# Kernel optimization log

Measured on AMD Instinct MI355X. Metric: run time of the kernel, lower is better.

## Reference

```python
import jax, jax.numpy as jnp
import numpy as np

N_NODES = 50000
N_EDGES = 800000
IN_FEATS = 256
N_HEADS = 4
OUT_FEATS = 32
NEG_SLOPE = 0.2


def setup_inputs() -> dict:
    key = jax.random.key(0)
    k_feat, k_src, k_dst, k_fc, k_al, k_ar, k_res = jax.random.split(key, 7)
    feat = jax.random.normal(k_feat, (N_NODES, IN_FEATS), dtype=jnp.float32)
    src = jax.random.randint(k_src, (N_EDGES,), 0, N_NODES)
    dst = jax.random.randint(k_dst, (N_EDGES,), 0, N_NODES)
    # xavier-normal-ish scales
    s_fc = (2.0 / (IN_FEATS + N_HEADS * OUT_FEATS)) ** 0.5
    W_fc = jax.random.normal(k_fc, (N_HEADS * OUT_FEATS, IN_FEATS), dtype=jnp.float32) * s_fc
    s_a = (2.0 / (1 + N_HEADS * OUT_FEATS)) ** 0.5
    attn_l = jax.random.normal(k_al, (N_HEADS, OUT_FEATS), dtype=jnp.float32) * s_a
    attn_r = jax.random.normal(k_ar, (N_HEADS, OUT_FEATS), dtype=jnp.float32) * s_a
    W_res = jax.random.normal(k_res, (N_HEADS * OUT_FEATS, IN_FEATS), dtype=jnp.float32) * s_fc
    return {"feat": feat, "src": src, "dst": dst, "W_fc": W_fc,
            "attn_l": attn_l, "attn_r": attn_r, "W_res": W_res}


def reference(feat, src, dst, W_fc, attn_l, attn_r, W_res):
    N = feat.shape[0]
    H, D = attn_l.shape
    ones_e = jnp.ones(src.shape[0], dtype=feat.dtype)

    # projection: [N, H, D]
    h = (feat @ W_fc.T).reshape(N, H, D)
    feat_dst = h  # dst features are pre-norm (torch code aliases before * norm)

    # symmetric norm on source side: out_degree^-0.5
    out_deg = jax.ops.segment_sum(ones_e, src, num_segments=N)
    feat_src = h * (jnp.clip(out_deg, 1.0) ** -0.5)[:, None, None]

    # per-node attention halves -> per-edge score, leaky relu
    el = jnp.einsum('nhd,hd->nh', feat_src, attn_l)  # [N, H]
    er = jnp.einsum('nhd,hd->nh', feat_dst, attn_r)  # [N, H]
    e = jax.nn.leaky_relu(el[src] + er[dst], NEG_SLOPE)  # [E, H]

    # edge_softmax over incoming edges of each dst node
    emax = jax.ops.segment_max(e, dst, num_segments=N)
    emax = jnp.where(jnp.isfinite(emax), emax, 0.0)  # guard empty segments
    ex = jnp.exp(e - emax[dst])
    denom = jax.ops.segment_sum(ex, dst, num_segments=N)
    a = ex / denom[dst]  # [E, H]

    # weighted scatter-sum of messages: u_mul_e + sum
    msg = feat_src[src] * a[:, :, None]  # [E, H, D]
    rst = jax.ops.segment_sum(msg, dst, num_segments=N)  # [N, H, D]

    # symmetric norm on destination side: in_degree^0.5
    in_deg = jax.ops.segment_sum(ones_e, dst, num_segments=N)
    rst = rst * jnp.sqrt(jnp.clip(in_deg, 1.0))[:, None, None]

    # residual projection
    rst = rst + (feat @ W_res.T).reshape(N, H, D)
    return rst
```

## Files before the change

kernel.cpp:

```cpp
#include <hip/hip_runtime.h>
#include <hip/hip_bf16.h>
#include <math.h>

#define HD 128
#define IN_F 256
#define NEG_SLOPE 0.2f
#define NMAX 50000

typedef __attribute__((ext_vector_type(8))) short short8;
typedef __attribute__((ext_vector_type(4))) float f32x4;

__device__ __forceinline__ unsigned short f2bf(float x) {
    __hip_bfloat16 b = __float2bfloat16(x);
    return *(unsigned short*)&b;
}
__device__ __forceinline__ float bf2f(unsigned short u) {
    unsigned int v = ((unsigned int)u) << 16;
    float f;
    __builtin_memcpy(&f, &v, 4);
    return f;
}

__global__ void cvt_w_kernel(const float4* __restrict__ wfc, const float4* __restrict__ wres,
                             ushort4* __restrict__ w16, int n4each) {
    int idx = blockIdx.x * blockDim.x + threadIdx.x;
    if (idx >= 2 * n4each) return;
    float4 f = (idx < n4each) ? wfc[idx] : wres[idx - n4each];
    ushort4 u;
    u.x = f2bf(f.x); u.y = f2bf(f.y); u.z = f2bf(f.z); u.w = f2bf(f.w);
    w16[idx] = u;
}

__global__ __launch_bounds__(512) void hist_kernel(const int* __restrict__ src,
                                                   const int* __restrict__ dst,
                                                   unsigned short* __restrict__ pc_src,
                                                   unsigned short* __restrict__ pc_dst,
                                                   int N, int E, int chunk) {
    __shared__ unsigned int h[NMAX / 2];
    int tid = threadIdx.x;
    int nh = N >> 1;
    uint4* h4 = (uint4*)h;
    for (int i = tid; i < (nh >> 2); i += 512) h4[i] = make_uint4(0, 0, 0, 0);
    for (int i = (nh & ~3) + tid; i < nh; i += 512) h[i] = 0;
    __syncthreads();

    const int* arr = blockIdx.y ? src : dst;
    int e1 = min(E, (int)(blockIdx.x + 1) * chunk);
    for (int e = blockIdx.x * chunk + tid; e < e1; e += 512) {
        int v = arr[e];
        atomicAdd(&h[v >> 1], 1u << ((v & 1) << 4));
    }
    __syncthreads();

    unsigned short* pc = (blockIdx.y ? pc_src : pc_dst) + (size_t)blockIdx.x * N;
    uint4* pc4 = (uint4*)pc;
    for (int i = tid; i < (nh >> 2); i += 512) pc4[i] = h4[i];
    for (int i = (nh & ~3) + tid; i < nh; i += 512) ((unsigned int*)pc)[i] = h[i];
}

__global__ __launch_bounds__(256) void sum_scan1_kernel(
    const unsigned short* __restrict__ pc_src, unsigned short* __restrict__ pc_dst,
    int* __restrict__ out_cnt, int* __restrict__ deg, int* __restrict__ bsum,
    int N, int C) {
    __shared__ int wsum[4];
    int n = blockIdx.x * 256 + threadIdx.x;
    int sd = 0;
    if (n < N) {
        int ss = 0;
        for (int c = 0; c < C; c++) {
            ss += pc_src[(size_t)c * N + n];
            unsigned short v = pc_dst[(size_t)c * N + n];
            pc_dst[(size_t)c * N + n] = (unsigned short)sd;
            sd += v;
        }
        out_cnt[n] = ss;
        deg[n] = sd;
    }
    int v = (n < N) ? sd : 0;
#pragma unroll
    for (int d = 1; d < 64; d <<= 1) v += __shfl_xor(v, d);
    if ((threadIdx.x & 63) == 0) wsum[threadIdx.x >> 6] = v;
    __syncthreads();
    if (threadIdx.x == 0) bsum[blockIdx.x] = wsum[0] + wsum[1] + wsum[2] + wsum[3];
}

__global__ __launch_bounds__(256) void scan2_kernel(int* __restrict__ bsum, int nb,
                                                    int* __restrict__ row_start_N, int E) {
    __shared__ int wtot[4];
    int tid = threadIdx.x, lane = tid & 63, wid = tid >> 6;
    int v = (tid < nb) ? bsum[tid] : 0;
    int incl = v;
#pragma unroll
    for (int d = 1; d < 64; d <<= 1) {
        int t = __shfl_up(incl, d);
        if (lane >= d) incl += t;
    }
    if (lane == 63) wtot[wid] = incl;
    __syncthreads();
    int woff = 0;
    for (int w = 0; w < wid; w++) woff += wtot[w];
    if (tid < nb) bsum[tid] = woff + incl - v;
    if (tid == 0) *row_start_N = E;
}

__global__ __launch_bounds__(256) void scan3_kernel(const int* __restrict__ deg,
                                                    const int* __restrict__ boff,
                                                    int* __restrict__ row_start, int N) {
    __shared__ int wsum[4];
    int i = blockIdx.x * 256 + threadIdx.x;
    int lane = threadIdx.x & 63, wid = threadIdx.x >> 6;
    int v = (i < N) ? deg[i] : 0;
    int incl = v;
#pragma unroll
    for (int d = 1; d < 64; d <<= 1) {
        int t = __shfl_up(incl, d);
        if (lane >= d) incl += t;
    }
    if (lane == 63) wsum[wid] = incl;
    __syncthreads();
    int woff = 0;
    for (int w = 0; w < wid; w++) woff += wsum[w];
    int excl = boff[blockIdx.x] + woff + incl - v;
    if (i < N) row_start[i] = excl;
}

__global__ __launch_bounds__(512) void place_kernel(const int* __restrict__ src,
                                                    const int* __restrict__ dst,
                                                    const unsigned short* __restrict__ chunkpre,
                                                    const int* __restrict__ row_start,
                                                    int* __restrict__ esrc,
                                                    int N, int E, int chunk) {
    __shared__ unsigned int cur[NMAX / 2];
    int tid = threadIdx.x;
    int nh = N >> 1;
    const unsigned short* cp = chunkpre + (size_t)blockIdx.x * N;
    const uint4* cp4 = (const uint4*)cp;
    uint4* cur4 = (uint4*)cur;
    for (int i = tid; i < (nh >> 2); i += 512) cur4[i] = cp4[i];
    for (int i = (nh & ~3) + tid; i < nh; i += 512) cur[i] = ((const unsigned int*)cp)[i];
    __syncthreads();

    int e1 = min(E, (int)(blockIdx.x + 1) * chunk);
    for (int e = blockIdx.x * chunk + tid; e < e1; e += 512) {
        int d = dst[e], s = src[e];
        int sh = (d & 1) << 4;
        unsigned int old = atomicAdd(&cur[d >> 1], 1u << sh);
        int rank = (old >> sh) & 0xffff;
        esrc[row_start[d] + rank] = s;
    }
}

__global__ __launch_bounds__(256) void gemm_fused(
    const float* __restrict__ feat, const __hip_bfloat16* __restrict__ w16,
    const int* __restrict__ out_cnt, const float* __restrict__ attn_l,
    const float* __restrict__ attn_r, unsigned short* __restrict__ h16,
    float* __restrict__ el, float* __restrict__ er, float* __restrict__ out, int N) {
    __shared__ unsigned short sA[32 * 256];
    int tid = threadIdx.x;
    int lane = tid & 63, wid = tid >> 6;
    int wn = wid;
    int bm = blockIdx.x * 32;
    int l15 = lane & 15, lg = lane >> 4;

#pragma unroll
    for (int i = 0; i < 4; i++) {
        int G = i * 256 + tid;
        int row = G >> 5, gc = G & 31;
        int gm = bm + row;
        gm = (gm < N) ? gm : (N - 1);
        const float4* fp = (const float4*)(feat + (size_t)gm * IN_F + gc * 8);
        float4 f0 = fp[0], f1 = fp[1];
        short8 v;
        v[0] = (short)f2bf(f0.x); v[1] = (short)f2bf(f0.y);
        v[2] = (short)f2bf(f0.z); v[3] = (short)f2bf(f0.w);
        v[4] = (short)f2bf(f1.x); v[5] = (short)f2bf(f1.y);
        v[6] = (short)f2bf(f1.z); v[7] = (short)f2bf(f1.w);
        *(short8*)&sA[row * 256 + ((gc ^ (row & 7)) * 8)] = v;
    }
    __syncthreads();

    int colbase = wn * 64;
    const __hip_bfloat16* bp[4];
#pragma unroll
    for (int ni = 0; ni < 4; ni++) {
        int c = colbase + ni * 16 + l15;
        bp[ni] = w16 + (size_t)c * IN_F + lg * 8;
    }

    f32x4 acc[2][4];
#pragma unroll
    for (int i = 0; i < 2; i++)
#pragma unroll
        for (int j = 0; j < 4; j++) acc[i][j] = (f32x4){0.f, 0.f, 0.f, 0.f};

#pragma unroll
    for (int k0 = 0; k0 < IN_F; k0 += 32) {
        short8 a[2], b[4];
#pragma unroll
        for (int mi = 0; mi < 2; mi++) {
            int row = mi * 16 + l15;
            int gs = ((k0 >> 3) + lg) ^ (row & 7);
            a[mi] = *(const short8*)&sA[row * 256 + gs * 8];
        }
#pragma unroll
        for (int ni = 0; ni < 4; ni++) b[ni] = *(const short8*)(bp[ni] + k0);
#pragma unroll
        for (int mi = 0; mi < 2; mi++)
#pragma unroll
            for (int ni = 0; ni < 4; ni++)
                acc[mi][ni] = __builtin_amdgcn_mfma_f32_16x16x32_bf16(
                    a[mi], b[ni], acc[mi][ni], 0, 0, 0);
    }

    bool isH = (wn < 2);
    int colloc = colbase & 127;
    float alv[4], arv[4];
    if (isH) {
#pragma unroll
        for (int ni = 0; ni < 4; ni++) {
            int c = colbase + ni * 16 + l15;
            alv[ni] = attn_l[c];
            arv[ni] = attn_r[c];
        }
    }
#pragma unroll
    for (int mi = 0; mi < 2; mi++) {
#pragma unroll
        for (int reg = 0; reg < 4; reg++) {
            int r = bm + mi * 16 + lg * 4 + reg;
            bool valid = (r < N);
            int rr = valid ? r : 0;
            if (isH) {
                float nrm = rsqrtf(fmaxf((float)out_cnt[rr], 1.0f));
                float pl0 = 0.f, pl1 = 0.f, pr0 = 0.f, pr1 = 0.f;
#pragma unroll
                for (int ni = 0; ni < 4; ni++) {
                    float v = acc[mi][ni][reg];
                    if (valid)
                        h16[(size_t)r * HD + colloc + ni * 16 + l15] = f2bf(v * nrm);
                    if (ni < 2) { pl0 += v * alv[ni]; pr0 += v * arv[ni]; }
                    else        { pl1 += v * alv[ni]; pr1 += v * arv[ni]; }
                }
                pl0 *= nrm; pl1 *= nrm;
#pragma unroll
                for (int m = 1; m < 16; m <<= 1) {
                    pl0 += __shfl_xor(pl0, m); pl1 += __shfl_xor(pl1, m);
                    pr0 += __shfl_xor(pr0, m); pr1 += __shfl_xor(pr1, m);
                }
                if (valid && (lane & 15) == 0) {
                    int hb = wn * 2;
                    el[r * 4 + hb] = pl0;     el[r * 4 + hb + 1] = pl1;
                    er[r * 4 + hb] = pr0;     er[r * 4 + hb + 1] = pr1;
                }
            } else if (valid) {
#pragma unroll
                for (int ni = 0; ni < 4; ni++)
                    out[(size_t)r * HD + colloc + ni * 16 + l15] = acc[mi][ni][reg];
            }
        }
    }
}

__global__ __launch_bounds__(256) void agg_kernel(const unsigned short* __restrict__ h16,
                                                  const float* __restrict__ el,
                                                  const float* __restrict__ er,
                                                  const int* __restrict__ row_start,
                                                  const int* __restrict__ esrc,
                                                  float* __restrict__ out, int N) {
    int wid = threadIdx.x >> 6, lane = threadIdx.x & 63;
    int n = blockIdx.x * 4 + wid;
    if (n >= N) return;
    int es = lane >> 4;
    int l15 = lane & 15;
    int h = l15 >> 2;
    int d0 = l15 * 8;
    int beg = row_start[n], end = row_start[n + 1];
    float erh = er[n * 4 + h];
    float den = 0.f;
    float acc[8];
#pragma unroll
    for (int j = 0; j < 8; j++) acc[j] = 0.f;

    for (int i = beg; i < end; i += 8) {
        int idx0 = i + es, idx1 = i + 4 + es;
        bool ok0 = idx0 < end, ok1 = idx1 < end;
        int s0 = esrc[ok0 ? idx0 : beg];
        int s1 = esrc[ok1 ? idx1 : beg];
        float ev0 = el[s0 * 4 + h];
        float ev1 = el[s1 * 4 + h];
        short8 hv0 = *(const short8*)(h16 + (size_t)s0 * HD + d0);
        short8 hv1 = *(const short8*)(h16 + (size_t)s1 * HD + d0);
        float e0 = ev0 + erh; e0 = (e0 > 0.f) ? e0 : NEG_SLOPE * e0;
        float e1 = ev1 + erh; e1 = (e1 > 0.f) ? e1 : NEG_SLOPE * e1;
        float ex0 = ok0 ? __expf(e0) : 0.f;
        float ex1 = ok1 ? __expf(e1) : 0.f;
        den += ex0 + ex1;
#pragma unroll
        for (int j = 0; j < 8; j++)
            acc[j] += ex0 * bf2f((unsigned short)hv0[j]) +
                      ex1 * bf2f((unsigned short)hv1[j]);
    }

#pragma unroll
    for (int m = 16; m < 64; m <<= 1) {
        den += __shfl_xor(den, m);
#pragma unroll
        for (int j = 0; j < 8; j++) acc[j] += __shfl_xor(acc[j], m);
    }

    if (es == 0) {
        float* op = out + (size_t)n * HD + d0;
        float4 r0 = *(const float4*)op;
        float4 r1 = *(const float4*)(op + 4);
        int indeg = end - beg;
        float sc = (indeg > 0) ? sqrtf((float)indeg) / den : 0.f;
        r0.x += sc * acc[0]; r0.y += sc * acc[1];
        r0.z += sc * acc[2]; r0.w += sc * acc[3];
        r1.x += sc * acc[4]; r1.y += sc * acc[5];
        r1.z += sc * acc[6]; r1.w += sc * acc[7];
        *(float4*)op = r0;
        *(float4*)(op + 4) = r1;
    }
}

extern "C" void kernel_launch(void* const* d_in, const int* in_sizes, int n_in,
                              void* d_out, int out_size, void* d_ws, size_t ws_size,
                              hipStream_t stream) {
    const float* feat   = (const float*)d_in[0];
    const int*   src    = (const int*)d_in[1];
    const int*   dst    = (const int*)d_in[2];
    const float* W_fc   = (const float*)d_in[3];
    const float* attn_l = (const float*)d_in[4];
    const float* attn_r = (const float*)d_in[5];
    const float* W_res  = (const float*)d_in[6];
    float* out = (float*)d_out;

    int N = in_sizes[0] / IN_F;
    int E = in_sizes[1];
    int nb = (N + 255) / 256;

    size_t off = 0;
    auto alloc = [&](size_t bytes) {
        size_t o = off;
        off = (off + bytes + 255) & ~(size_t)255;
        return o;
    };
    char* ws = (char*)d_ws;
    unsigned short* h16 = (unsigned short*)(ws + alloc((size_t)N * HD * 2));
    __hip_bfloat16* w16 = (__hip_bfloat16*)(ws + alloc((size_t)2 * HD * IN_F * 2));
    float* el           = (float*)(ws + alloc((size_t)N * 4 * 4));
    float* er           = (float*)(ws + alloc((size_t)N * 4 * 4));
    int* out_cnt        = (int*)(ws + alloc((size_t)N * 4));
    int* deg            = (int*)(ws + alloc((size_t)N * 4));
    int* row_start      = (int*)(ws + alloc((size_t)(N + 1) * 4));
    int* bsum           = (int*)(ws + alloc((size_t)nb * 4));
    int* esrc           = (int*)(ws + alloc((size_t)E * 4));

    size_t per_chunk = (size_t)4 * N;
    size_t avail = (ws_size > off + 4096) ? (ws_size - off - 4096) : 0;
    int C = (int)(avail / per_chunk);
    if (C > 128) C = 128;
    if (C < 32) C = 32;
    unsigned short* pc_dst = (unsigned short*)(ws + alloc((size_t)C * N * 2));
    unsigned short* pc_src = (unsigned short*)(ws + alloc((size_t)C * N * 2));
    int chunk = (E + C - 1) / C;

    int n4each = HD * IN_F / 4;
    cvt_w_kernel<<<(2 * n4each + 255) / 256, 256, 0, stream>>>(
        (const float4*)W_fc, (const float4*)W_res, (ushort4*)w16, n4each);

    hist_kernel<<<dim3(C, 2), 512, 0, stream>>>(src, dst, pc_src, pc_dst, N, E, chunk);
    sum_scan1_kernel<<<nb, 256, 0, stream>>>(pc_src, pc_dst, out_cnt, deg, bsum, N, C);
    scan2_kernel<<<1, 256, 0, stream>>>(bsum, nb, row_start + N, E);
    scan3_kernel<<<nb, 256, 0, stream>>>(deg, bsum, row_start, N);
    place_kernel<<<C, 512, 0, stream>>>(src, dst, pc_dst, row_start, esrc, N, E, chunk);

    gemm_fused<<<(N + 31) / 32, 256, 0, stream>>>(feat, (const __hip_bfloat16*)w16,
                                                  out_cnt, attn_l, attn_r,
                                                  h16, el, er, out, N);

    int nb4 = (N + 3) / 4;
    agg_kernel<<<nb4, 256, 0, stream>>>(h16, el, er, row_start, esrc, out, N);
}
```

Baseline: 157.2 us.

## Make projection GEMM persistent with register-resident weights and prefetched A tiles

Turns the fused projection GEMM into a persistent kernel with a fixed grid of 512 blocks that loop over 32-row tiles. Each wave loads its weight slice into registers once, instead of reloading B from global memory for every tile. The next tile's feature rows are prefetched into registers while the current tile is computed, and LDS is double-buffered. The cost is heavy register pressure from 32 short8 weight registers per lane, which could cap occupancy or cause spills, and fewer blocks to spread across CUs.

```diff
diff --git a/kernel.cpp b/kernel.cpp
--- a/kernel.cpp
+++ b/kernel.cpp
@@ -6,6 +6,7 @@
 #define IN_F 256
 #define NEG_SLOPE 0.2f
 #define NMAX 50000
+#define GEMM_BLOCKS 512
 
 typedef __attribute__((ext_vector_type(8))) short short8;
 typedef __attribute__((ext_vector_type(4))) float f32x4;
@@ -150,66 +151,25 @@
     }
 }
 
-__global__ __launch_bounds__(256) void gemm_fused(
+__global__ __launch_bounds__(256, 2) void gemm_fused(
     const float* __restrict__ feat, const __hip_bfloat16* __restrict__ w16,
     const int* __restrict__ out_cnt, const float* __restrict__ attn_l,
     const float* __restrict__ attn_r, unsigned short* __restrict__ h16,
-    float* __restrict__ el, float* __restrict__ er, float* __restrict__ out, int N) {
-    __shared__ unsigned short sA[32 * 256];
+    float* __restrict__ el, float* __restrict__ er, float* __restrict__ out,
+    int N, int ntiles) {
+    __shared__ unsigned short sA[2][32 * 256];
     int tid = threadIdx.x;
-    int lane = tid & 63, wid = tid >> 6;
-    int wn = wid;
-    int bm = blockIdx.x * 32;
+    int lane = tid & 63, wn = tid >> 6;
     int l15 = lane & 15, lg = lane >> 4;
-
-#pragma unroll
-    for (int i = 0; i < 4; i++) {
-        int G = i * 256 + tid;
-        int row = G >> 5, gc = G & 31;
-        int gm = bm + row;
-        gm = (gm < N) ? gm : (N - 1);
-        const float4* fp = (const float4*)(feat + (size_t)gm * IN_F + gc * 8);
-        float4 f0 = fp[0], f1 = fp[1];
-        short8 v;
-        v[0] = (short)f2bf(f0.x); v[1] = (short)f2bf(f0.y);
-        v[2] = (short)f2bf(f0.z); v[3] = (short)f2bf(f0.w);
-        v[4] = (short)f2bf(f1.x); v[5] = (short)f2bf(f1.y);
-        v[6] = (short)f2bf(f1.z); v[7] = (short)f2bf(f1.w);
-        *(short8*)&sA[row * 256 + ((gc ^ (row & 7)) * 8)] = v;
-    }
-    __syncthreads();
-
     int colbase = wn * 64;
-    const __hip_bfloat16* bp[4];
+
+    short8 breg[4][8];
 #pragma unroll
     for (int ni = 0; ni < 4; ni++) {
-        int c = colbase + ni * 16 + l15;
-        bp[ni] = w16 + (size_t)c * IN_F + lg * 8;
-    }
-
-    f32x4 acc[2][4];
-#pragma unroll
-    for (int i = 0; i < 2; i++)
-#pragma unroll
-        for (int j = 0; j < 4; j++) acc[i][j] = (f32x4){0.f, 0.f, 0.f, 0.f};
-
-#pragma unroll
-    for (int k0 = 0; k0 < IN_F; k0 += 32) {
-        short8 a[2], b[4];
-#pragma unroll
-        for (int mi = 0; mi < 2; mi++) {
-            int row = mi * 16 + l15;
-            int gs = ((k0 >> 3) + lg) ^ (row & 7);
-            a[mi] = *(const short8*)&sA[row * 256 + gs * 8];
-        }
-#pragma unroll
-        for (int ni = 0; ni < 4; ni++) b[ni] = *(const short8*)(bp[ni] + k0);
-#pragma unroll
-        for (int mi = 0; mi < 2; mi++)
-#pragma unroll
-            for (int ni = 0; ni < 4; ni++)
-                acc[mi][ni] = __builtin_amdgcn_mfma_f32_16x16x32_bf16(
-                    a[mi], b[ni], acc[mi][ni], 0, 0, 0);
+        const __hip_bfloat16* bp = w16 + (size_t)(colbase + ni * 16 + l15) * IN_F + lg * 8;
+#pragma unroll
+        for (int kk = 0; kk < 8; kk++)
+            breg[ni][kk] = *(const short8*)(bp + kk * 32);
     }
 
     bool isH = (wn < 2);
@@ -223,41 +183,110 @@
             arv[ni] = attn_r[c];
         }
     }
-#pragma unroll
-    for (int mi = 0; mi < 2; mi++) {
-#pragma unroll
-        for (int reg = 0; reg < 4; reg++) {
-            int r = bm + mi * 16 + lg * 4 + reg;
-            bool valid = (r < N);
-            int rr = valid ? r : 0;
-            if (isH) {
-                float nrm = rsqrtf(fmaxf((float)out_cnt[rr], 1.0f));
-                float pl0 = 0.f, pl1 = 0.f, pr0 = 0.f, pr1 = 0.f;
-#pragma unroll
-                for (int ni = 0; ni < 4; ni++) {
-                    float v = acc[mi][ni][reg];
-                    if (valid)
-                        h16[(size_t)r * HD + colloc + ni * 16 + l15] = f2bf(v * nrm);
-                    if (ni < 2) { pl0 += v * alv[ni]; pr0 += v * arv[ni]; }
-                    else        { pl1 += v * alv[ni]; pr1 += v * arv[ni]; }
+
+    int srow[4], sgc[4];
+#pragma unroll
+    for (int i = 0; i < 4; i++) {
+        int G = i * 256 + tid;
+        srow[i] = G >> 5;
+        sgc[i] = G & 31;
+    }
+
+    float4 fA[4][2];
+    int t = blockIdx.x;
+#pragma unroll
+    for (int i = 0; i < 4; i++) {
+        int gm = t * 32 + srow[i];
+        gm = (gm < N) ? gm : (N - 1);
+        const float4* fp = (const float4*)(feat + (size_t)gm * IN_F + sgc[i] * 8);
+        fA[i][0] = fp[0];
+        fA[i][1] = fp[1];
+    }
+
+    int cur = 0;
+    for (; t < ntiles; t += GEMM_BLOCKS) {
+#pragma unroll
+        for (int i = 0; i < 4; i++) {
+            short8 v;
+            v[0] = (short)f2bf(fA[i][0].x); v[1] = (short)f2bf(fA[i][0].y);
+            v[2] = (short)f2bf(fA[i][0].z); v[3] = (short)f2bf(fA[i][0].w);
+            v[4] = (short)f2bf(fA[i][1].x); v[5] = (short)f2bf(fA[i][1].y);
+            v[6] = (short)f2bf(fA[i][1].z); v[7] = (short)f2bf(fA[i][1].w);
+            *(short8*)&sA[cur][srow[i] * 256 + ((sgc[i] ^ (srow[i] & 7)) * 8)] = v;
+        }
+        int tn = t + GEMM_BLOCKS;
+        if (tn < ntiles) {
+#pragma unroll
+            for (int i = 0; i < 4; i++) {
+                int gm = tn * 32 + srow[i];
+                gm = (gm < N) ? gm : (N - 1);
+                const float4* fp = (const float4*)(feat + (size_t)gm * IN_F + sgc[i] * 8);
+                fA[i][0] = fp[0];
+                fA[i][1] = fp[1];
+            }
+        }
+        __syncthreads();
+
+        f32x4 acc[2][4];
+#pragma unroll
+        for (int i = 0; i < 2; i++)
+#pragma unroll
+            for (int j = 0; j < 4; j++) acc[i][j] = (f32x4){0.f, 0.f, 0.f, 0.f};
+#pragma unroll
+        for (int kk = 0; kk < 8; kk++) {
+            short8 a[2];
+#pragma unroll
+            for (int mi = 0; mi < 2; mi++) {
+                int row = mi * 16 + l15;
+                int gs = (kk * 4 + lg) ^ (row & 7);
+                a[mi] = *(const short8*)&sA[cur][row * 256 + gs * 8];
+            }
+#pragma unroll
+            for (int mi = 0; mi < 2; mi++)
+#pragma unroll
+                for (int ni = 0; ni < 4; ni++)
+                    acc[mi][ni] = __builtin_amdgcn_mfma_f32_16x16x32_bf16(
+                        a[mi], breg[ni][kk], acc[mi][ni], 0, 0, 0);
+        }
+
+        int bm = t * 32;
+#pragma unroll
+        for (int mi = 0; mi < 2; mi++) {
+#pragma unroll
+            for (int reg = 0; reg < 4; reg++) {
+                int r = bm + mi * 16 + lg * 4 + reg;
+                bool valid = (r < N);
+                int rr = valid ? r : 0;
+                if (isH) {
+                    float nrm = rsqrtf(fmaxf((float)out_cnt[rr], 1.0f));
+                    float pl0 = 0.f, pl1 = 0.f, pr0 = 0.f, pr1 = 0.f;
+#pragma unroll
+                    for (int ni = 0; ni < 4; ni++) {
+                        float v = acc[mi][ni][reg];
+                        if (valid)
+                            h16[(size_t)r * HD + colloc + ni * 16 + l15] = f2bf(v * nrm);
+                        if (ni < 2) { pl0 += v * alv[ni]; pr0 += v * arv[ni]; }
+                        else        { pl1 += v * alv[ni]; pr1 += v * arv[ni]; }
+                    }
+                    pl0 *= nrm; pl1 *= nrm;
+#pragma unroll
+                    for (int m = 1; m < 16; m <<= 1) {
+                        pl0 += __shfl_xor(pl0, m); pl1 += __shfl_xor(pl1, m);
+                        pr0 += __shfl_xor(pr0, m); pr1 += __shfl_xor(pr1, m);
+                    }
+                    if (valid && (lane & 15) == 0) {
+                        int hb = wn * 2;
+                        el[r * 4 + hb] = pl0;     el[r * 4 + hb + 1] = pl1;
+                        er[r * 4 + hb] = pr0;     er[r * 4 + hb + 1] = pr1;
+                    }
+                } else if (valid) {
+#pragma unroll
+                    for (int ni = 0; ni < 4; ni++)
+                        out[(size_t)r * HD + colloc + ni * 16 + l15] = acc[mi][ni][reg];
                 }
-                pl0 *= nrm; pl1 *= nrm;
-#pragma unroll
-                for (int m = 1; m < 16; m <<= 1) {
-                    pl0 += __shfl_xor(pl0, m); pl1 += __shfl_xor(pl1, m);
-                    pr0 += __shfl_xor(pr0, m); pr1 += __shfl_xor(pr1, m);
-                }
-                if (valid && (lane & 15) == 0) {
-                    int hb = wn * 2;
-                    el[r * 4 + hb] = pl0;     el[r * 4 + hb + 1] = pl1;
-                    er[r * 4 + hb] = pr0;     er[r * 4 + hb + 1] = pr1;
-                }
-            } else if (valid) {
-#pragma unroll
-                for (int ni = 0; ni < 4; ni++)
-                    out[(size_t)r * HD + colloc + ni * 16 + l15] = acc[mi][ni][reg];
             }
         }
+        cur ^= 1;
     }
 }
 
@@ -375,9 +404,10 @@
     scan3_kernel<<<nb, 256, 0, stream>>>(deg, bsum, row_start, N);
     place_kernel<<<C, 512, 0, stream>>>(src, dst, pc_dst, row_start, esrc, N, E, chunk);
 
-    gemm_fused<<<(N + 31) / 32, 256, 0, stream>>>(feat, (const __hip_bfloat16*)w16,
-                                                  out_cnt, attn_l, attn_r,
-                                                  h16, el, er, out, N);
+    int ntiles = (N + 31) / 32;
+    gemm_fused<<<GEMM_BLOCKS, 256, 0, stream>>>(feat, (const __hip_bfloat16*)w16,
+                                                out_cnt, attn_l, attn_r,
+                                                h16, el, er, out, N, ntiles);
 
     int nb4 = (N + 3) / 4;
     agg_kernel<<<nb4, 256, 0, stream>>>(h16, el, er, row_start, esrc, out, N);
```

New measurement: 149.1 us. -5.2%, faster.

## Drop GEMM shared staging, keep residual in bf16, software-pipeline aggregation gathers

Applied to the files above, without the earlier changes.

The GEMM kernel no longer stages the feature tile through shared memory. Each wave loads its feat rows straight from global memory and keeps all weight fragments in registers, which removes the shared-memory copy and the barrier. The residual projection is written as a bf16 buffer instead of into fp32 out, so agg reads the residual at half the bytes and writes out only once rather than doing a read-modify-write. The aggregation loop now prefetches the next batch of edge gathers before computing the current one to hide memory latency. This adds bf16 rounding to the residual path and more register pressure, and the four waves per block now each load the same feat rows redundantly.

```diff
diff --git a/kernel.cpp b/kernel.cpp
--- a/kernel.cpp
+++ b/kernel.cpp
@@ -19,6 +19,14 @@
     float f;
     __builtin_memcpy(&f, &v, 4);
     return f;
+}
+__device__ __forceinline__ short8 pack8(float4 f0, float4 f1) {
+    short8 v;
+    v[0] = (short)f2bf(f0.x); v[1] = (short)f2bf(f0.y);
+    v[2] = (short)f2bf(f0.z); v[3] = (short)f2bf(f0.w);
+    v[4] = (short)f2bf(f1.x); v[5] = (short)f2bf(f1.y);
+    v[6] = (short)f2bf(f1.z); v[7] = (short)f2bf(f1.w);
+    return v;
 }
 
 __global__ void cvt_w_kernel(const float4* __restrict__ wfc, const float4* __restrict__ wres,
@@ -154,37 +162,29 @@
     const float* __restrict__ feat, const __hip_bfloat16* __restrict__ w16,
     const int* __restrict__ out_cnt, const float* __restrict__ attn_l,
     const float* __restrict__ attn_r, unsigned short* __restrict__ h16,
-    float* __restrict__ el, float* __restrict__ er, float* __restrict__ out, int N) {
-    __shared__ unsigned short sA[32 * 256];
+    float* __restrict__ el, float* __restrict__ er,
+    unsigned short* __restrict__ resid16, int N) {
     int tid = threadIdx.x;
-    int lane = tid & 63, wid = tid >> 6;
-    int wn = wid;
+    int lane = tid & 63, wn = tid >> 6;
+    int l15 = lane & 15, lg = lane >> 4;
+    int colbase = wn * 64;
     int bm = blockIdx.x * 32;
-    int l15 = lane & 15, lg = lane >> 4;
-
-#pragma unroll
-    for (int i = 0; i < 4; i++) {
-        int G = i * 256 + tid;
-        int row = G >> 5, gc = G & 31;
-        int gm = bm + row;
-        gm = (gm < N) ? gm : (N - 1);
-        const float4* fp = (const float4*)(feat + (size_t)gm * IN_F + gc * 8);
-        float4 f0 = fp[0], f1 = fp[1];
-        short8 v;
-        v[0] = (short)f2bf(f0.x); v[1] = (short)f2bf(f0.y);
-        v[2] = (short)f2bf(f0.z); v[3] = (short)f2bf(f0.w);
-        v[4] = (short)f2bf(f1.x); v[5] = (short)f2bf(f1.y);
-        v[6] = (short)f2bf(f1.z); v[7] = (short)f2bf(f1.w);
-        *(short8*)&sA[row * 256 + ((gc ^ (row & 7)) * 8)] = v;
-    }
-    __syncthreads();
-
-    int colbase = wn * 64;
-    const __hip_bfloat16* bp[4];
+
+    short8 breg[4][8];
 #pragma unroll
     for (int ni = 0; ni < 4; ni++) {
-        int c = colbase + ni * 16 + l15;
-        bp[ni] = w16 + (size_t)c * IN_F + lg * 8;
+        const __hip_bfloat16* bp = w16 + (size_t)(colbase + ni * 16 + l15) * IN_F + lg * 8;
+#pragma unroll
+        for (int kk = 0; kk < 8; kk++)
+            breg[ni][kk] = *(const short8*)(bp + kk * 32);
+    }
+
+    const float* arow[2];
+#pragma unroll
+    for (int mi = 0; mi < 2; mi++) {
+        int r = bm + mi * 16 + l15;
+        r = (r < N) ? r : (N - 1);
+        arow[mi] = feat + (size_t)r * IN_F + lg * 8;
     }
 
     f32x4 acc[2][4];
@@ -194,22 +194,20 @@
         for (int j = 0; j < 4; j++) acc[i][j] = (f32x4){0.f, 0.f, 0.f, 0.f};
 
 #pragma unroll
-    for (int k0 = 0; k0 < IN_F; k0 += 32) {
-        short8 a[2], b[4];
+    for (int kk = 0; kk < 8; kk++) {
+        short8 a[2];
 #pragma unroll
         for (int mi = 0; mi < 2; mi++) {
-            int row = mi * 16 + l15;
-            int gs = ((k0 >> 3) + lg) ^ (row & 7);
-            a[mi] = *(const short8*)&sA[row * 256 + gs * 8];
-        }
-#pragma unroll
-        for (int ni = 0; ni < 4; ni++) b[ni] = *(const short8*)(bp[ni] + k0);
+            float4 f0 = *(const float4*)(arow[mi] + kk * 32);
+            float4 f1 = *(const float4*)(arow[mi] + kk * 32 + 4);
+            a[mi] = pack8(f0, f1);
+        }
 #pragma unroll
         for (int mi = 0; mi < 2; mi++)
 #pragma unroll
             for (int ni = 0; ni < 4; ni++)
                 acc[mi][ni] = __builtin_amdgcn_mfma_f32_16x16x32_bf16(
-                    a[mi], b[ni], acc[mi][ni], 0, 0, 0);
+                    a[mi], breg[ni][kk], acc[mi][ni], 0, 0, 0);
     }
 
     bool isH = (wn < 2);
@@ -255,7 +253,8 @@
             } else if (valid) {
 #pragma unroll
                 for (int ni = 0; ni < 4; ni++)
-                    out[(size_t)r * HD + colloc + ni * 16 + l15] = acc[mi][ni][reg];
+                    resid16[(size_t)r * HD + colloc + ni * 16 + l15] =
+                        f2bf(acc[mi][ni][reg]);
             }
         }
     }
@@ -266,6 +265,7 @@
                                                   const float* __restrict__ er,
                                                   const int* __restrict__ row_start,
                                                   const int* __restrict__ esrc,
+                                                  const unsigned short* __restrict__ resid16,
                                                   float* __restrict__ out, int N) {
     int wid = threadIdx.x >> 6, lane = threadIdx.x & 63;
     int n = blockIdx.x * 4 + wid;
@@ -281,15 +281,38 @@
 #pragma unroll
     for (int j = 0; j < 8; j++) acc[j] = 0.f;
 
-    for (int i = beg; i < end; i += 8) {
-        int idx0 = i + es, idx1 = i + 4 + es;
-        bool ok0 = idx0 < end, ok1 = idx1 < end;
-        int s0 = esrc[ok0 ? idx0 : beg];
-        int s1 = esrc[ok1 ? idx1 : beg];
-        float ev0 = el[s0 * 4 + h];
-        float ev1 = el[s1 * 4 + h];
-        short8 hv0 = *(const short8*)(h16 + (size_t)s0 * HD + d0);
-        short8 hv1 = *(const short8*)(h16 + (size_t)s1 * HD + d0);
+    if (beg < end) {
+        int s0, s1; bool ok0, ok1;
+        float ev0, ev1; short8 hv0, hv1;
+        {
+            int i0 = beg + es, i1 = beg + 4 + es;
+            ok0 = i0 < end; ok1 = i1 < end;
+            s0 = esrc[ok0 ? i0 : beg];
+            s1 = esrc[ok1 ? i1 : beg];
+            ev0 = el[s0 * 4 + h]; ev1 = el[s1 * 4 + h];
+            hv0 = *(const short8*)(h16 + (size_t)s0 * HD + d0);
+            hv1 = *(const short8*)(h16 + (size_t)s1 * HD + d0);
+        }
+        for (int base = beg + 8; base < end; base += 8) {
+            int i0 = base + es, i1 = base + 4 + es;
+            bool p0 = i0 < end, p1 = i1 < end;
+            int t0 = esrc[p0 ? i0 : beg];
+            int t1 = esrc[p1 ? i1 : beg];
+            float fv0 = el[t0 * 4 + h];
+            float fv1 = el[t1 * 4 + h];
+            short8 g0 = *(const short8*)(h16 + (size_t)t0 * HD + d0);
+            short8 g1 = *(const short8*)(h16 + (size_t)t1 * HD + d0);
+            float e0 = ev0 + erh; e0 = (e0 > 0.f) ? e0 : NEG_SLOPE * e0;
+            float e1 = ev1 + erh; e1 = (e1 > 0.f) ? e1 : NEG_SLOPE * e1;
+            float ex0 = ok0 ? __expf(e0) : 0.f;
+            float ex1 = ok1 ? __expf(e1) : 0.f;
+            den += ex0 + ex1;
+#pragma unroll
+            for (int j = 0; j < 8; j++)
+                acc[j] += ex0 * bf2f((unsigned short)hv0[j]) +
+                          ex1 * bf2f((unsigned short)hv1[j]);
+            ok0 = p0; ok1 = p1; ev0 = fv0; ev1 = fv1; hv0 = g0; hv1 = g1;
+        }
         float e0 = ev0 + erh; e0 = (e0 > 0.f) ? e0 : NEG_SLOPE * e0;
         float e1 = ev1 + erh; e1 = (e1 > 0.f) ? e1 : NEG_SLOPE * e1;
         float ex0 = ok0 ? __expf(e0) : 0.f;
@@ -309,17 +332,17 @@
     }
 
     if (es == 0) {
-        float* op = out + (size_t)n * HD + d0;
-        float4 r0 = *(const float4*)op;
-        float4 r1 = *(const float4*)(op + 4);
+        const unsigned short* rp = resid16 + (size_t)n * HD + d0;
+        short8 rv = *(const short8*)rp;
         int indeg = end - beg;
         float sc = (indeg > 0) ? sqrtf((float)indeg) / den : 0.f;
-        r0.x += sc * acc[0]; r0.y += sc * acc[1];
-        r0.z += sc * acc[2]; r0.w += sc * acc[3];
-        r1.x += sc * acc[4]; r1.y += sc * acc[5];
-        r1.z += sc * acc[6]; r1.w += sc * acc[7];
-        *(float4*)op = r0;
-        *(float4*)(op + 4) = r1;
+        float o[8];
+#pragma unroll
+        for (int j = 0; j < 8; j++)
+            o[j] = sc * acc[j] + bf2f((unsigned short)rv[j]);
+        float* op = out + (size_t)n * HD + d0;
+        *(float4*)op = make_float4(o[0], o[1], o[2], o[3]);
+        *(float4*)(op + 4) = make_float4(o[4], o[5], o[6], o[7]);
     }
 }
 
@@ -346,15 +369,16 @@
         return o;
     };
     char* ws = (char*)d_ws;
-    unsigned short* h16 = (unsigned short*)(ws + alloc((size_t)N * HD * 2));
-    __hip_bfloat16* w16 = (__hip_bfloat16*)(ws + alloc((size_t)2 * HD * IN_F * 2));
-    float* el           = (float*)(ws + alloc((size_t)N * 4 * 4));
-    float* er           = (float*)(ws + alloc((size_t)N * 4 * 4));
-    int* out_cnt        = (int*)(ws + alloc((size_t)N * 4));
-    int* deg            = (int*)(ws + alloc((size_t)N * 4));
-    int* row_start      = (int*)(ws + alloc((size_t)(N + 1) * 4));
-    int* bsum           = (int*)(ws + alloc((size_t)nb * 4));
-    int* esrc           = (int*)(ws + alloc((size_t)E * 4));
+    unsigned short* h16     = (unsigned short*)(ws + alloc((size_t)N * HD * 2));
+    unsigned short* resid16 = (unsigned short*)(ws + alloc((size_t)N * HD * 2));
+    __hip_bfloat16* w16     = (__hip_bfloat16*)(ws + alloc((size_t)2 * HD * IN_F * 2));
+    float* el               = (float*)(ws + alloc((size_t)N * 4 * 4));
+    float* er               = (float*)(ws + alloc((size_t)N * 4 * 4));
+    int* out_cnt            = (int*)(ws + alloc((size_t)N * 4));
+    int* deg                = (int*)(ws + alloc((size_t)N * 4));
+    int* row_start          = (int*)(ws + alloc((size_t)(N + 1) * 4));
+    int* bsum               = (int*)(ws + alloc((size_t)nb * 4));
+    int* esrc               = (int*)(ws + alloc((size_t)E * 4));
 
     size_t per_chunk = (size_t)4 * N;
     size_t avail = (ws_size > off + 4096) ? (ws_size - off - 4096) : 0;
@@ -377,8 +401,8 @@
 
     gemm_fused<<<(N + 31) / 32, 256, 0, stream>>>(feat, (const __hip_bfloat16*)w16,
                                                   out_cnt, attn_l, attn_r,
-                                                  h16, el, er, out, N);
+                                                  h16, el, er, resid16, N);
 
     int nb4 = (N + 3) / 4;
-    agg_kernel<<<nb4, 256, 0, stream>>>(h16, el, er, row_start, esrc, out, N);
-}
+    agg_kernel<<<nb4, 256, 0, stream>>>(h16, el, er, row_start, esrc, resid16, out, N);
+}
```

Result: slower. 172.6 us (+9.8%).
